# Kernel tuning notes

Hardware: AMD Instinct MI355X
Metric: run time of the kernel (lower is better)

The kernel has to match this reference:

```python
import jax, jax.numpy as jnp
import numpy as np

TEMPERATURE = 0.07
EPS = 1e-8  # F.cosine_similarity eps


def setup_inputs() -> dict:
    key = jax.random.key(0)
    k1, k2, k3, k4 = jax.random.split(key, 4)
    N, D, M, C = 4096, 1024, 8192, 100
    q = jax.random.normal(k1, (N, D), dtype=jnp.float32)
    labels = jax.random.randint(k2, (N,), 0, C, dtype=jnp.int32)
    memory_logits = jax.random.normal(k3, (N, M), dtype=jnp.float32)
    memory_targets = jax.random.bernoulli(k4, 0.5, (N, M)).astype(jnp.float32)
    return {"q": q, "labels": labels, "memory_logits": memory_logits,
            "memory_targets": memory_targets}


def reference(q, labels, memory_logits, memory_targets):
    N = q.shape[0]
    # cosine similarity as normalize + GEMM (second operand detached, as in torch)
    qn = q / jnp.maximum(jnp.linalg.norm(q, axis=-1, keepdims=True), EPS)
    sims = qn @ jax.lax.stop_gradient(qn).T               # [N, N]
    src_contrast = sims / TEMPERATURE
    logits_max = jax.lax.stop_gradient(
        jnp.max(src_contrast, axis=1, keepdims=True))
    src_logits = src_contrast - logits_max                # [N, N]
    # positive-pair mask with self excluded
    src_targets = (labels[:, None] == labels[None, :]).astype(jnp.float32)
    self_mask = 1.0 - jnp.eye(N, dtype=jnp.float32)
    src_targets = src_targets * self_mask
    targets = jnp.concatenate([src_targets, memory_targets], axis=1)  # [N, N+M]
    src_exp_logits = jnp.exp(src_logits) * self_mask
    logits = jnp.concatenate([src_logits, memory_logits], axis=1)     # [N, N+M]
    denom = src_exp_logits.sum(axis=1) + jnp.exp(memory_logits).sum(axis=1)
    log_prob = logits - jnp.log(denom)[:, None]
    mean_log_prob_pos = (targets * log_prob).sum(axis=1) / targets.sum(axis=1)
    return -jnp.mean(mean_log_prob_pos)
```

## Files before the change

### kernel.cpp

```cpp
#include <hip/hip_runtime.h>
#include <hip/hip_bf16.h>
#include <math.h>

typedef unsigned short u16;
typedef __bf16 bf16x8 __attribute__((ext_vector_type(8)));
typedef float f32x4 __attribute__((ext_vector_type(4)));
typedef unsigned short u16x4 __attribute__((ext_vector_type(4)));

#define NROW 4096
#define KDIM 1024
#define MDIM 8192
#define TILE 128
#define BK 64
#define NCT (NROW / TILE)

__device__ __forceinline__ u16 f2bf(float x) {
    unsigned int u = __float_as_uint(x);
    unsigned int r = (u + 0x7fffu + ((u >> 16) & 1u)) >> 16;
    return (u16)r;
}

__device__ __forceinline__ void gload16(const u16* g, u16* l) {
    __builtin_amdgcn_global_load_lds(
        (const __attribute__((address_space(1))) void*)g,
        (__attribute__((address_space(3))) void*)l,
        16, 0, 0);
}

__global__ void k_normalize(const float* __restrict__ q, u16* __restrict__ qn) {
    const int r = blockIdx.x;
    const int t = threadIdx.x;
    const int lane = t & 63, wid = t >> 6;
    const float4* qr = (const float4*)(q + (size_t)r * KDIM);
    float4 v = qr[t];
    float ss = v.x * v.x + v.y * v.y + v.z * v.z + v.w * v.w;
    #pragma unroll
    for (int d = 1; d < 64; d <<= 1) ss += __shfl_xor(ss, d);
    __shared__ float red[4];
    if (lane == 0) red[wid] = ss;
    __syncthreads();
    float tot = red[0] + red[1] + red[2] + red[3];
    float nrm = sqrtf(tot);
    float inv = 1.0f / fmaxf(nrm, 1e-8f);
    u16x4 o;
    o[0] = f2bf(v.x * inv); o[1] = f2bf(v.y * inv);
    o[2] = f2bf(v.z * inv); o[3] = f2bf(v.w * inv);
    *(u16x4*)(qn + (size_t)r * KDIM + t * 4) = o;
}

__global__ void k_memstats(const float* __restrict__ ml, const float* __restrict__ mt,
                           float4* __restrict__ out) {
    const int r = blockIdx.x;
    const int t = threadIdx.x;
    const int lane = t & 63, wid = t >> 6;
    const float4* pl = (const float4*)(ml + (size_t)r * MDIM);
    const float4* pt = (const float4*)(mt + (size_t)r * MDIM);
    float S2 = 0.f, dot = 0.f, smt = 0.f;
    #pragma unroll
    for (int it = 0; it < MDIM / 4 / 256; ++it) {
        int idx = it * 256 + t;
        float4 l = pl[idx];
        float4 m = pt[idx];
        S2 += __expf(l.x) + __expf(l.y) + __expf(l.z) + __expf(l.w);
        dot += m.x * l.x + m.y * l.y + m.z * l.z + m.w * l.w;
        smt += m.x + m.y + m.z + m.w;
    }
    #pragma unroll
    for (int d = 1; d < 64; d <<= 1) {
        S2  += __shfl_xor(S2, d);
        dot += __shfl_xor(dot, d);
        smt += __shfl_xor(smt, d);
    }
    __shared__ float red[4][3];
    if (lane == 0) { red[wid][0] = S2; red[wid][1] = dot; red[wid][2] = smt; }
    __syncthreads();
    if (t == 0) {
        out[r] = make_float4(red[0][0] + red[1][0] + red[2][0] + red[3][0],
                             red[0][1] + red[1][1] + red[2][1] + red[3][1],
                             red[0][2] + red[1][2] + red[2][2] + red[3][2], 0.f);
    }
}

__global__ void k_gemm_stats(const u16* __restrict__ qn, const int* __restrict__ labels,
                             float4* __restrict__ partials) {
    __shared__ u16 ldsA[TILE * BK];
    __shared__ u16 ldsB[TILE * BK];
    __shared__ int labR[TILE], labC[TILE];

    const int ct = blockIdx.x, bi = blockIdx.y;
    const int t = threadIdx.x;
    const int w = t >> 6, lane = t & 63;
    const int rowbase = bi * TILE, colbase = ct * TILE;

    if (t < 128) labR[t] = labels[rowbase + t];
    else labC[t - 128] = labels[colbase + (t - 128)];

    const int wr = (w >> 1) * 64, wc = (w & 1) * 64;
    const int cl = lane & 15, cg = lane >> 4;

    const int sr = lane >> 3;
    const int skb = lane & 7;

    f32x4 acc[4][4];
    #pragma unroll
    for (int i = 0; i < 4; ++i)
        #pragma unroll
        for (int j = 0; j < 4; ++j)
            acc[i][j] = {0.f, 0.f, 0.f, 0.f};

    for (int ks = 0; ks < KDIM / BK; ++ks) {
        const int k0 = ks * BK;
        #pragma unroll
        for (int it = 0; it < 4; ++it) {
            int c = w * 4 + it;
            int rr = c * 8 + sr;
            const u16* ga = qn + (size_t)(rowbase + rr) * KDIM + k0 + skb * 8;
            gload16(ga, ldsA + c * 512);
            const u16* gb = qn + (size_t)(colbase + rr) * KDIM + k0 + skb * 8;
            gload16(gb, ldsB + c * 512);
        }
        asm volatile("s_waitcnt vmcnt(0)" ::: "memory");
        __syncthreads();
        #pragma unroll
        for (int k2 = 0; k2 < 2; ++k2) {
            bf16x8 a[4], b[4];
            #pragma unroll
            for (int f = 0; f < 4; ++f) {
                a[f] = *(const bf16x8*)&ldsA[(wr + f * 16 + cl) * BK + k2 * 32 + cg * 8];
                b[f] = *(const bf16x8*)&ldsB[(wc + f * 16 + cl) * BK + k2 * 32 + cg * 8];
            }
            #pragma unroll
            for (int fm = 0; fm < 4; ++fm)
                #pragma unroll
                for (int fn = 0; fn < 4; ++fn)
                    acc[fm][fn] = __builtin_amdgcn_mfma_f32_16x16x32_bf16(
                        a[fm], b[fn], acc[fm][fn], 0, 0, 0);
        }
        __syncthreads();
    }

    const float invT = (float)(1.0 / 0.07);
    #pragma unroll
    for (int fm = 0; fm < 4; ++fm) {
        #pragma unroll
        for (int reg = 0; reg < 4; ++reg) {
            const int lr = wr + fm * 16 + cg * 4 + reg;
            const int gi = rowbase + lr;
            const int li = labR[lr];
            float c0 = acc[fm][0][reg] * invT;
            float c1 = acc[fm][1][reg] * invT;
            float c2 = acc[fm][2][reg] * invT;
            float c3 = acc[fm][3][reg] * invT;
            float m = fmaxf(fmaxf(c0, c1), fmaxf(c2, c3));
            #pragma unroll
            for (int d = 1; d < 16; d <<= 1) m = fmaxf(m, __shfl_xor(m, d));
            float se = 0.f, ps = 0.f, cnt = 0.f;
            #pragma unroll
            for (int fn = 0; fn < 4; ++fn) {
                float c = (fn == 0) ? c0 : (fn == 1) ? c1 : (fn == 2) ? c2 : c3;
                const int lc = wc + fn * 16 + cl;
                const int gj = colbase + lc;
                const bool self = (gj == gi);
                se += self ? 0.f : __expf(c - m);
                const bool pos = (!self) && (labC[lc] == li);
                ps += pos ? c : 0.f;
                cnt += pos ? 1.f : 0.f;
            }
            #pragma unroll
            for (int d = 1; d < 16; d <<= 1) {
                se  += __shfl_xor(se, d);
                ps  += __shfl_xor(ps, d);
                cnt += __shfl_xor(cnt, d);
            }
            if (cl == 0) partials[(size_t)ct * NROW + gi] = make_float4(m, se, ps, cnt);
        }
    }
}

__global__ void k_combine(const float4* __restrict__ partials, const float4* __restrict__ ms,
                          float* __restrict__ vals) {
    const int r = blockIdx.x * blockDim.x + threadIdx.x;
    if (r >= NROW) return;
    float M = -3.4e38f;
    #pragma unroll 4
    for (int ct = 0; ct < NCT; ++ct) M = fmaxf(M, partials[(size_t)ct * NROW + r].x);
    float S1 = 0.f, ps = 0.f, cnt = 0.f;
    #pragma unroll 4
    for (int ct = 0; ct < NCT; ++ct) {
        float4 p = partials[(size_t)ct * NROW + r];
        S1 += p.y * __expf(p.x - M);
        ps += p.z;
        cnt += p.w;
    }
    float4 m = ms[r];
    float L = logf(S1 + m.x);
    float val = (ps - cnt * (M + L) + m.y - m.z * L) / (cnt + m.z);
    vals[r] = val;
}

__global__ void k_finalize(const float* __restrict__ vals, float* __restrict__ out) {
    const int t = threadIdx.x;
    const int lane = t & 63, wid = t >> 6;
    float s = 0.f;
    for (int i = t; i < NROW; i += 256) s += vals[i];
    #pragma unroll
    for (int d = 1; d < 64; d <<= 1) s += __shfl_xor(s, d);
    __shared__ float red[4];
    if (lane == 0) red[wid] = s;
    __syncthreads();
    if (t == 0) out[0] = -(red[0] + red[1] + red[2] + red[3]) * (1.0f / (float)NROW);
}

extern "C" void kernel_launch(void* const* d_in, const int* in_sizes, int n_in,
                              void* d_out, int out_size, void* d_ws, size_t ws_size,
                              hipStream_t stream) {
    const float* q  = (const float*)d_in[0];
    const int* labels = (const int*)d_in[1];
    const float* ml = (const float*)d_in[2];
    const float* mt = (const float*)d_in[3];
    float* out = (float*)d_out;

    char* w = (char*)d_ws;
    u16* qn          = (u16*)w;
    float4* partials = (float4*)(w + 8388608);
    float4* memstats = (float4*)(w + 10485760);
    float* vals      = (float*)(w + 10551296);

    k_normalize<<<NROW, 256, 0, stream>>>(q, qn);
    k_memstats<<<NROW, 256, 0, stream>>>(ml, mt, memstats);
    k_gemm_stats<<<dim3(NCT, NROW / TILE), 256, 0, stream>>>(qn, labels, partials);
    k_combine<<<NROW / 256, 256, 0, stream>>>(partials, memstats, vals);
    k_finalize<<<1, 256, 0, stream>>>(vals, out);
}
```

Measured before the change: 114.3 us.

## Fuse memory-stats reduction into GEMM kernel with interleaved block roles

Merges the memory-logit statistics pass and the similarity GEMM into one launch. Block indices are interleaved so that every fifth block runs a GEMM tile and the other four each reduce one memory row, letting the bandwidth-bound streaming overlap the MFMA-bound tiles. The memory reduction now writes per-wave partials instead of a block-level shared-memory reduction, and the combine kernel sums them. The cost is higher register and LDS pressure from the shared kernel footprint, which may lower occupancy for the streaming blocks.

```diff
diff --git a/kernel.cpp b/kernel.cpp
--- a/kernel.cpp
+++ b/kernel.cpp
@@ -13,6 +13,8 @@
 #define TILE 128
 #define BK 64
 #define NCT (NROW / TILE)
+#define NGEMM (NCT * (NROW / TILE))
+#define NMEM  NROW
 
 __device__ __forceinline__ u16 f2bf(float x) {
     unsigned int u = __float_as_uint(x);
@@ -48,48 +50,46 @@
     *(u16x4*)(qn + (size_t)r * KDIM + t * 4) = o;
 }
 
-__global__ void k_memstats(const float* __restrict__ ml, const float* __restrict__ mt,
-                           float4* __restrict__ out) {
-    const int r = blockIdx.x;
-    const int t = threadIdx.x;
-    const int lane = t & 63, wid = t >> 6;
-    const float4* pl = (const float4*)(ml + (size_t)r * MDIM);
-    const float4* pt = (const float4*)(mt + (size_t)r * MDIM);
-    float S2 = 0.f, dot = 0.f, smt = 0.f;
-    #pragma unroll
-    for (int it = 0; it < MDIM / 4 / 256; ++it) {
-        int idx = it * 256 + t;
-        float4 l = pl[idx];
-        float4 m = pt[idx];
-        S2 += __expf(l.x) + __expf(l.y) + __expf(l.z) + __expf(l.w);
-        dot += m.x * l.x + m.y * l.y + m.z * l.z + m.w * l.w;
-        smt += m.x + m.y + m.z + m.w;
-    }
-    #pragma unroll
-    for (int d = 1; d < 64; d <<= 1) {
-        S2  += __shfl_xor(S2, d);
-        dot += __shfl_xor(dot, d);
-        smt += __shfl_xor(smt, d);
-    }
-    __shared__ float red[4][3];
-    if (lane == 0) { red[wid][0] = S2; red[wid][1] = dot; red[wid][2] = smt; }
-    __syncthreads();
-    if (t == 0) {
-        out[r] = make_float4(red[0][0] + red[1][0] + red[2][0] + red[3][0],
-                             red[0][1] + red[1][1] + red[2][1] + red[3][1],
-                             red[0][2] + red[1][2] + red[2][2] + red[3][2], 0.f);
-    }
-}
-
-__global__ void k_gemm_stats(const u16* __restrict__ qn, const int* __restrict__ labels,
-                             float4* __restrict__ partials) {
+__global__ void k_fused(const u16* __restrict__ qn, const int* __restrict__ labels,
+                        const float* __restrict__ ml, const float* __restrict__ mt,
+                        float4* __restrict__ partials, float4* __restrict__ memq) {
     __shared__ u16 ldsA[TILE * BK];
     __shared__ u16 ldsB[TILE * BK];
     __shared__ int labR[TILE], labC[TILE];
 
-    const int ct = blockIdx.x, bi = blockIdx.y;
+    const int bid = blockIdx.x;
     const int t = threadIdx.x;
     const int w = t >> 6, lane = t & 63;
+    const int g = bid / 5, rem = bid % 5;
+
+    if (rem != 4) {
+        const int r = g * 4 + rem;
+        const float4* pl = (const float4*)(ml + (size_t)r * MDIM);
+        const float4* pt = (const float4*)(mt + (size_t)r * MDIM);
+        const int base = w * 512 + lane;
+        float4 L[8], T[8];
+        #pragma unroll
+        for (int j = 0; j < 8; ++j) L[j] = pl[base + j * 64];
+        #pragma unroll
+        for (int j = 0; j < 8; ++j) T[j] = pt[base + j * 64];
+        float S2 = 0.f, dot = 0.f, smt = 0.f;
+        #pragma unroll
+        for (int j = 0; j < 8; ++j) {
+            S2  += __expf(L[j].x) + __expf(L[j].y) + __expf(L[j].z) + __expf(L[j].w);
+            dot += T[j].x * L[j].x + T[j].y * L[j].y + T[j].z * L[j].z + T[j].w * L[j].w;
+            smt += T[j].x + T[j].y + T[j].z + T[j].w;
+        }
+        #pragma unroll
+        for (int d = 1; d < 64; d <<= 1) {
+            S2  += __shfl_xor(S2, d);
+            dot += __shfl_xor(dot, d);
+            smt += __shfl_xor(smt, d);
+        }
+        if (lane == 0) memq[r * 4 + w] = make_float4(S2, dot, smt, 0.f);
+        return;
+    }
+
+    const int ct = g & 31, bi = g >> 5;
     const int rowbase = bi * TILE, colbase = ct * TILE;
 
     if (t < 128) labR[t] = labels[rowbase + t];
@@ -177,7 +177,7 @@
     }
 }
 
-__global__ void k_combine(const float4* __restrict__ partials, const float4* __restrict__ ms,
+__global__ void k_combine(const float4* __restrict__ partials, const float4* __restrict__ memq,
                           float* __restrict__ vals) {
     const int r = blockIdx.x * blockDim.x + threadIdx.x;
     if (r >= NROW) return;
@@ -192,9 +192,14 @@
         ps += p.z;
         cnt += p.w;
     }
-    float4 m = ms[r];
-    float L = logf(S1 + m.x);
-    float val = (ps - cnt * (M + L) + m.y - m.z * L) / (cnt + m.z);
+    float S2 = 0.f, mdot = 0.f, smt = 0.f;
+    #pragma unroll
+    for (int k = 0; k < 4; ++k) {
+        float4 mq = memq[r * 4 + k];
+        S2 += mq.x; mdot += mq.y; smt += mq.z;
+    }
+    float L = logf(S1 + S2);
+    float val = (ps - cnt * (M + L) + mdot - smt * L) / (cnt + smt);
     vals[r] = val;
 }
 
@@ -223,12 +228,11 @@
     char* w = (char*)d_ws;
     u16* qn          = (u16*)w;
     float4* partials = (float4*)(w + 8388608);
-    float4* memstats = (float4*)(w + 10485760);
-    float* vals      = (float*)(w + 10551296);
+    float4* memq     = (float4*)(w + 10485760);
+    float* vals      = (float*)(w + 10747904);
 
     k_normalize<<<NROW, 256, 0, stream>>>(q, qn);
-    k_memstats<<<NROW, 256, 0, stream>>>(ml, mt, memstats);
-    k_gemm_stats<<<dim3(NCT, NROW / TILE), 256, 0, stream>>>(qn, labels, partials);
-    k_combine<<<NROW / 256, 256, 0, stream>>>(partials, memstats, vals);
+    k_fused<<<NGEMM + NMEM, 256, 0, stream>>>(qn, labels, ml, mt, partials, memq);
+    k_combine<<<NROW / 256, 256, 0, stream>>>(partials, memq, vals);
     k_finalize<<<1, 256, 0, stream>>>(vals, out);
 }
```

New measurement: 123.0 us. 1.08x slower.

## Exploit symmetry of Gram matrix: compute only upper-triangle tiles

Applied to the files above, without the earlier changes.

Because the normalized similarity matrix is symmetric, the GEMM now launches only upper-triangular tile pairs and, for off-diagonal tiles, also derives column-wise softmax statistics that serve as row statistics of the mirrored tile. The partial-stat buffer is split per half-tile segment (twice as many segments), and the combine step iterates over them. The memstats loop is also unrolled to issue more loads per iteration. This roughly halves GEMM work at the cost of a heavier epilogue, a larger combine pass and a small tile-index decode loop.

```diff
diff --git a/kernel.cpp b/kernel.cpp
--- a/kernel.cpp
+++ b/kernel.cpp
@@ -12,7 +12,9 @@
 #define MDIM 8192
 #define TILE 128
 #define BK 64
-#define NCT (NROW / TILE)
+#define NT   (NROW / TILE)
+#define NSEG (NT * 2)
+#define NTRI (NT * (NT + 1) / 2)
 
 __device__ __forceinline__ u16 f2bf(float x) {
     unsigned int u = __float_as_uint(x);
@@ -40,8 +42,7 @@
     if (lane == 0) red[wid] = ss;
     __syncthreads();
     float tot = red[0] + red[1] + red[2] + red[3];
-    float nrm = sqrtf(tot);
-    float inv = 1.0f / fmaxf(nrm, 1e-8f);
+    float inv = 1.0f / fmaxf(sqrtf(tot), 1e-8f);
     u16x4 o;
     o[0] = f2bf(v.x * inv); o[1] = f2bf(v.y * inv);
     o[2] = f2bf(v.z * inv); o[3] = f2bf(v.w * inv);
@@ -57,13 +58,20 @@
     const float4* pt = (const float4*)(mt + (size_t)r * MDIM);
     float S2 = 0.f, dot = 0.f, smt = 0.f;
     #pragma unroll
-    for (int it = 0; it < MDIM / 4 / 256; ++it) {
-        int idx = it * 256 + t;
-        float4 l = pl[idx];
-        float4 m = pt[idx];
-        S2 += __expf(l.x) + __expf(l.y) + __expf(l.z) + __expf(l.w);
-        dot += m.x * l.x + m.y * l.y + m.z * l.z + m.w * l.w;
-        smt += m.x + m.y + m.z + m.w;
+    for (int it = 0; it < 2; ++it) {
+        const int i0 = it * 1024 + t;
+        float4 l0 = pl[i0], l1 = pl[i0 + 256], l2 = pl[i0 + 512], l3 = pl[i0 + 768];
+        float4 t0 = pt[i0], t1 = pt[i0 + 256], t2 = pt[i0 + 512], t3 = pt[i0 + 768];
+        S2 += __expf(l0.x) + __expf(l0.y) + __expf(l0.z) + __expf(l0.w);
+        S2 += __expf(l1.x) + __expf(l1.y) + __expf(l1.z) + __expf(l1.w);
+        S2 += __expf(l2.x) + __expf(l2.y) + __expf(l2.z) + __expf(l2.w);
+        S2 += __expf(l3.x) + __expf(l3.y) + __expf(l3.z) + __expf(l3.w);
+        dot += t0.x * l0.x + t0.y * l0.y + t0.z * l0.z + t0.w * l0.w;
+        dot += t1.x * l1.x + t1.y * l1.y + t1.z * l1.z + t1.w * l1.w;
+        dot += t2.x * l2.x + t2.y * l2.y + t2.z * l2.z + t2.w * l2.w;
+        dot += t3.x * l3.x + t3.y * l3.y + t3.z * l3.z + t3.w * l3.w;
+        smt += t0.x + t0.y + t0.z + t0.w + t1.x + t1.y + t1.z + t1.w;
+        smt += t2.x + t2.y + t2.z + t2.w + t3.x + t3.y + t3.z + t3.w;
     }
     #pragma unroll
     for (int d = 1; d < 64; d <<= 1) {
@@ -74,20 +82,22 @@
     __shared__ float red[4][3];
     if (lane == 0) { red[wid][0] = S2; red[wid][1] = dot; red[wid][2] = smt; }
     __syncthreads();
-    if (t == 0) {
+    if (t == 0)
         out[r] = make_float4(red[0][0] + red[1][0] + red[2][0] + red[3][0],
                              red[0][1] + red[1][1] + red[2][1] + red[3][1],
                              red[0][2] + red[1][2] + red[2][2] + red[3][2], 0.f);
-    }
-}
-
-__global__ void k_gemm_stats(const u16* __restrict__ qn, const int* __restrict__ labels,
-                             float4* __restrict__ partials) {
+}
+
+__global__ void k_gemm_sym(const u16* __restrict__ qn, const int* __restrict__ labels,
+                           float4* __restrict__ partials) {
     __shared__ u16 ldsA[TILE * BK];
     __shared__ u16 ldsB[TILE * BK];
     __shared__ int labR[TILE], labC[TILE];
 
-    const int ct = blockIdx.x, bi = blockIdx.y;
+    int u = blockIdx.x, bi = 0;
+    while (u >= NT - bi) { u -= NT - bi; ++bi; }
+    const int ct = bi + u;
+
     const int t = threadIdx.x;
     const int w = t >> 6, lane = t & 63;
     const int rowbase = bi * TILE, colbase = ct * TILE;
@@ -97,9 +107,7 @@
 
     const int wr = (w >> 1) * 64, wc = (w & 1) * 64;
     const int cl = lane & 15, cg = lane >> 4;
-
-    const int sr = lane >> 3;
-    const int skb = lane & 7;
+    const int sr = lane >> 3, skb = lane & 7;
 
     f32x4 acc[4][4];
     #pragma unroll
@@ -114,10 +122,8 @@
         for (int it = 0; it < 4; ++it) {
             int c = w * 4 + it;
             int rr = c * 8 + sr;
-            const u16* ga = qn + (size_t)(rowbase + rr) * KDIM + k0 + skb * 8;
-            gload16(ga, ldsA + c * 512);
-            const u16* gb = qn + (size_t)(colbase + rr) * KDIM + k0 + skb * 8;
-            gload16(gb, ldsB + c * 512);
+            gload16(qn + (size_t)(rowbase + rr) * KDIM + k0 + skb * 8, ldsA + c * 512);
+            gload16(qn + (size_t)(colbase + rr) * KDIM + k0 + skb * 8, ldsB + c * 512);
         }
         asm volatile("s_waitcnt vmcnt(0)" ::: "memory");
         __syncthreads();
@@ -140,6 +146,7 @@
     }
 
     const float invT = (float)(1.0 / 0.07);
+
     #pragma unroll
     for (int fm = 0; fm < 4; ++fm) {
         #pragma unroll
@@ -159,8 +166,7 @@
             for (int fn = 0; fn < 4; ++fn) {
                 float c = (fn == 0) ? c0 : (fn == 1) ? c1 : (fn == 2) ? c2 : c3;
                 const int lc = wc + fn * 16 + cl;
-                const int gj = colbase + lc;
-                const bool self = (gj == gi);
+                const bool self = (colbase + lc == gi);
                 se += self ? 0.f : __expf(c - m);
                 const bool pos = (!self) && (labC[lc] == li);
                 ps += pos ? c : 0.f;
@@ -172,30 +178,66 @@
                 ps  += __shfl_xor(ps, d);
                 cnt += __shfl_xor(cnt, d);
             }
-            if (cl == 0) partials[(size_t)ct * NROW + gi] = make_float4(m, se, ps, cnt);
-        }
-    }
-}
-
-__global__ void k_combine(const float4* __restrict__ partials, const float4* __restrict__ ms,
+            if (cl == 0)
+                partials[(size_t)(ct * 2 + (w & 1)) * NROW + gi] =
+                    make_float4(m, se, ps, cnt);
+        }
+    }
+
+    if (bi != ct) {
+        #pragma unroll
+        for (int fn = 0; fn < 4; ++fn) {
+            const int lc = wc + fn * 16 + cl;
+            const int gj = colbase + lc;
+            const int lj = labC[lc];
+            float m = -3.4e38f;
+            #pragma unroll
+            for (int fm = 0; fm < 4; ++fm)
+                #pragma unroll
+                for (int reg = 0; reg < 4; ++reg)
+                    m = fmaxf(m, acc[fm][fn][reg] * invT);
+            m = fmaxf(m, __shfl_xor(m, 16));
+            m = fmaxf(m, __shfl_xor(m, 32));
+            float se = 0.f, ps = 0.f, cnt = 0.f;
+            #pragma unroll
+            for (int fm = 0; fm < 4; ++fm) {
+                #pragma unroll
+                for (int reg = 0; reg < 4; ++reg) {
+                    float c = acc[fm][fn][reg] * invT;
+                    const int lr = wr + fm * 16 + cg * 4 + reg;
+                    se += __expf(c - m);
+                    const bool pos = (labR[lr] == lj);
+                    ps += pos ? c : 0.f;
+                    cnt += pos ? 1.f : 0.f;
+                }
+            }
+            se += __shfl_xor(se, 16); ps += __shfl_xor(ps, 16); cnt += __shfl_xor(cnt, 16);
+            se += __shfl_xor(se, 32); ps += __shfl_xor(ps, 32); cnt += __shfl_xor(cnt, 32);
+            if (cg == 0)
+                partials[(size_t)(bi * 2 + (w >> 1)) * NROW + gj] =
+                    make_float4(m, se, ps, cnt);
+        }
+    }
+}
+
+__global__ void k_combine(const float4* __restrict__ partials, const float4* __restrict__ memq,
                           float* __restrict__ vals) {
     const int r = blockIdx.x * blockDim.x + threadIdx.x;
     if (r >= NROW) return;
     float M = -3.4e38f;
-    #pragma unroll 4
-    for (int ct = 0; ct < NCT; ++ct) M = fmaxf(M, partials[(size_t)ct * NROW + r].x);
+    #pragma unroll 8
+    for (int s = 0; s < NSEG; ++s) M = fmaxf(M, partials[(size_t)s * NROW + r].x);
     float S1 = 0.f, ps = 0.f, cnt = 0.f;
-    #pragma unroll 4
-    for (int ct = 0; ct < NCT; ++ct) {
-        float4 p = partials[(size_t)ct * NROW + r];
+    #pragma unroll 8
+    for (int s = 0; s < NSEG; ++s) {
+        float4 p = partials[(size_t)s * NROW + r];
         S1 += p.y * __expf(p.x - M);
         ps += p.z;
         cnt += p.w;
     }
-    float4 m = ms[r];
-    float L = logf(S1 + m.x);
-    float val = (ps - cnt * (M + L) + m.y - m.z * L) / (cnt + m.z);
-    vals[r] = val;
+    float4 mq = memq[r];
+    float L = logf(S1 + mq.x);
+    vals[r] = (ps - cnt * (M + L) + mq.y - mq.z * L) / (cnt + mq.z);
 }
 
 __global__ void k_finalize(const float* __restrict__ vals, float* __restrict__ out) {
@@ -223,12 +265,12 @@
     char* w = (char*)d_ws;
     u16* qn          = (u16*)w;
     float4* partials = (float4*)(w + 8388608);
-    float4* memstats = (float4*)(w + 10485760);
-    float* vals      = (float*)(w + 10551296);
+    float4* memq     = (float4*)(w + 12582912);
+    float* vals      = (float*)(w + 12648448);
 
     k_normalize<<<NROW, 256, 0, stream>>>(q, qn);
-    k_memstats<<<NROW, 256, 0, stream>>>(ml, mt, memstats);
-    k_gemm_stats<<<dim3(NCT, NROW / TILE), 256, 0, stream>>>(qn, labels, partials);
-    k_combine<<<NROW / 256, 256, 0, stream>>>(partials, memstats, vals);
+    k_memstats<<<NROW, 256, 0, stream>>>(ml, mt, memq);
+    k_gemm_sym<<<NTRI, 256, 0, stream>>>(qn, labels, partials);
+    k_combine<<<NROW / 256, 256, 0, stream>>>(partials, memq, vals);
     k_finalize<<<1, 256, 0, stream>>>(vals, out);
 }
```

After: 111.4 us. -2.6%, faster.
